# Kernel optimization log

Measured on AMD Instinct MI355X. Metric: run time of the kernel, lower is better.

## Reference

```python
import jax, jax.numpy as jnp
import numpy as np

B, S, D, H, MLP = 8, 1024, 768, 12, 3072
HD = D // H
EPS = 1e-5


def setup_inputs() -> dict:
    key = jax.random.key(0)
    ks = jax.random.split(key, 5)
    sd = lambda fan_in: 1.0 / np.sqrt(fan_in)
    return {
        "x": jax.random.normal(ks[0], (B, S, D), jnp.float32),
        "w_qkv": jax.random.normal(ks[1], (D, 3 * D), jnp.float32) * sd(D),
        "w_out": jax.random.normal(ks[2], (D, D), jnp.float32) * sd(D),
        "b_out": jnp.zeros((D,), jnp.float32),
        "w1": jax.random.normal(ks[3], (D, MLP), jnp.float32) * sd(D),
        "b1": jnp.zeros((MLP,), jnp.float32),
        "w2": jax.random.normal(ks[4], (MLP, D), jnp.float32) * sd(MLP),
        "b2": jnp.zeros((D,), jnp.float32),
    }


def _instance_norm(x):
    # torch InstanceNorm2d on a 3D [B,S,D] tensor treats it as unbatched (C,H,W):
    # normalize over (S, D) per batch element, biased var, eps=1e-5, no affine.
    mu = jnp.mean(x, axis=(1, 2), keepdims=True)
    var = jnp.mean(jnp.square(x - mu), axis=(1, 2), keepdims=True)
    return (x - mu) * jax.lax.rsqrt(var + EPS)


def reference(x, w_qkv, w_out, b_out, w1, b1, w2, b2):
    scale = HD ** -0.5
    # --- self-attention branch ---
    h = _instance_norm(x)
    qkv = (h @ w_qkv).reshape(B, S, 3, H, HD)          # (qkv, heads, head_dim) split
    qkv = qkv.transpose(2, 0, 3, 1, 4)                  # [3, B, H, S, HD]
    q, k, v = qkv[0], qkv[1], qkv[2]
    att = jax.nn.softmax(jnp.einsum('bhxd,bhyd->bhxy', q, k) * scale, axis=-1)
    o = jnp.einsum('bhxy,bhyd->bhxd', att, v)           # [B, H, S, HD]
    o = o.transpose(0, 2, 1, 3).reshape(B, S, D)        # b h l d -> b l (h d)
    x = x + (o @ w_out + b_out)
    # --- MLP branch (exact erf GELU, as nn.GELU default) ---
    h2 = _instance_norm(x)
    m = jax.nn.gelu(h2 @ w1 + b1, approximate=False) @ w2 + b2
    return x + m
```

## Files before the change

kernel.cpp:

```cpp
#include <hip/hip_runtime.h>
#include <hip/hip_bf16.h>

typedef __hip_bfloat16 bf16;
typedef __attribute__((ext_vector_type(8))) short short8;
typedef __attribute__((ext_vector_type(4))) float f32x4;

#define B_   8
#define S_   1024
#define D_   768
#define H_   12
#define HD_  64
#define MLP_ 3072
#define SD_  (S_ * D_)

#define QSCALE 0.18033688011112042f

__device__ __forceinline__ float b2f(short h) {
  union { unsigned u; float f; } w;
  w.u = ((unsigned)(unsigned short)h) << 16;
  return w.f;
}

__device__ __forceinline__ void gl2lds16(const bf16* g, bf16* l) {
  __builtin_amdgcn_global_load_lds(
      (const __attribute__((address_space(1))) unsigned*)(const void*)g,
      (__attribute__((address_space(3))) unsigned*)(void*)l, 16, 0, 0);
}

__global__ __launch_bounds__(256) void transpose_all(
    const float* __restrict__ w_qkv, const float* __restrict__ w_out,
    const float* __restrict__ w1, const float* __restrict__ w2,
    bf16* __restrict__ t_qkv, bf16* __restrict__ t_out,
    bf16* __restrict__ t1, bf16* __restrict__ t2) {
  const int t = blockIdx.x;
  const float* in; bf16* out; int R, C, idx;
  if (t < 1728)      { in = w_qkv; out = t_qkv; R = 768;  C = 2304; idx = t; }
  else if (t < 2304) { in = w_out; out = t_out; R = 768;  C = 768;  idx = t - 1728; }
  else if (t < 4608) { in = w1;    out = t1;    R = 768;  C = 3072; idx = t - 2304; }
  else               { in = w2;    out = t2;    R = 3072; C = 768;  idx = t - 4608; }
  const int nbx = C >> 5;
  const int bx = (idx % nbx) * 32, by = (idx / nbx) * 32;
  __shared__ float tt[32][33];
  const int tx = threadIdx.x & 31, ty = threadIdx.x >> 5;
#pragma unroll
  for (int rr = 0; rr < 32; rr += 8)
    tt[ty + rr][tx] = in[(long)(by + ty + rr) * C + bx + tx];
  __syncthreads();
#pragma unroll
  for (int rr = 0; rr < 32; rr += 8)
    out[(long)(bx + ty + rr) * R + by + tx] = __float2bfloat16(tt[tx][ty + rr]);
}

__global__ __launch_bounds__(256) void stats_partial(const float* __restrict__ x,
                                                     float* __restrict__ redp,
                                                     const bf16* __restrict__ wt1,
                                                     const bf16* __restrict__ wt_qkv,
                                                     float* __restrict__ cs1,
                                                     float* __restrict__ csq,
                                                     bf16* __restrict__ xb) {
  if (blockIdx.x >= 768) {
    const bf16* wsrc; float* cdst; int bi;
    if (blockIdx.x < 816) { wsrc = wt1;    cdst = cs1; bi = blockIdx.x - 768; }
    else                  { wsrc = wt_qkv; cdst = csq; bi = blockIdx.x - 816; }
    const int row = bi * 64 + (threadIdx.x >> 2);
    const int part = threadIdx.x & 3;
    const bf16* wr = wsrc + (long)row * 768 + part * 192;
    float s = 0.f;
#pragma unroll
    for (int u = 0; u < 24; ++u) {
      short8 v = *(const short8*)(wr + u * 8);
#pragma unroll
      for (int e = 0; e < 8; ++e) s += b2f(v[e]);
    }
    s += __shfl_xor(s, 1, 64);
    s += __shfl_xor(s, 2, 64);
    if (part == 0) cdst[row] = s;
    return;
  }
  const long off = (long)blockIdx.x * 8192;
  float s = 0.f, s2 = 0.f;
#pragma unroll
  for (int it = 0; it < 4; ++it) {
    const long i = off + ((long)threadIdx.x + it * 256) * 8;
    float4 v0 = *(const float4*)(x + i);
    float4 v1 = *(const float4*)(x + i + 4);
    s += v0.x + v0.y + v0.z + v0.w + v1.x + v1.y + v1.z + v1.w;
    s2 += v0.x * v0.x + v0.y * v0.y + v0.z * v0.z + v0.w * v0.w +
          v1.x * v1.x + v1.y * v1.y + v1.z * v1.z + v1.w * v1.w;
    __align__(16) bf16 tmp[8];
    tmp[0] = __float2bfloat16(v0.x); tmp[1] = __float2bfloat16(v0.y);
    tmp[2] = __float2bfloat16(v0.z); tmp[3] = __float2bfloat16(v0.w);
    tmp[4] = __float2bfloat16(v1.x); tmp[5] = __float2bfloat16(v1.y);
    tmp[6] = __float2bfloat16(v1.z); tmp[7] = __float2bfloat16(v1.w);
    *(short8*)(xb + i) = *(const short8*)tmp;
  }
#pragma unroll
  for (int o = 1; o < 64; o <<= 1) { s += __shfl_xor(s, o, 64); s2 += __shfl_xor(s2, o, 64); }
  __shared__ float sh[8];
  const int wave = threadIdx.x >> 6, lane = threadIdx.x & 63;
  if (lane == 0) { sh[wave * 2] = s; sh[wave * 2 + 1] = s2; }
  __syncthreads();
  if (threadIdx.x == 0) {
    redp[blockIdx.x * 2]     = sh[0] + sh[2] + sh[4] + sh[6];
    redp[blockIdx.x * 2 + 1] = sh[1] + sh[3] + sh[5] + sh[7];
  }
}

__global__ __launch_bounds__(512) void stats_final(const float* __restrict__ redp,
                                                   float* __restrict__ red_x,
                                                   float* __restrict__ red2) {
  const int b = threadIdx.x >> 6, lane = threadIdx.x & 63;
  const int i0 = (b * 96 + lane) * 2;
  float s  = redp[i0]     + ((lane < 32) ? redp[i0 + 128]     : 0.f);
  float s2 = redp[i0 + 1] + ((lane < 32) ? redp[i0 + 128 + 1] : 0.f);
#pragma unroll
  for (int o = 1; o < 64; o <<= 1) { s += __shfl_xor(s, o, 64); s2 += __shfl_xor(s2, o, 64); }
  if (lane == 0) { red_x[b * 2] = s; red_x[b * 2 + 1] = s2; }
  if (threadIdx.x < 16) red2[threadIdx.x] = 0.f;
}

template <int EPI, bool STATS>
__global__ __launch_bounds__(256) void gemm_k(
    const bf16* __restrict__ A, const bf16* __restrict__ Bt,
    int M, int N, int K,
    const float* __restrict__ biasf, const float* __restrict__ resf,
    const float* __restrict__ cs, const float* __restrict__ stat_in,
    float* __restrict__ outf,
    bf16* __restrict__ outb0, bf16* __restrict__ outb1, bf16* __restrict__ outb2,
    float* __restrict__ statp) {
  __shared__ __align__(16) bf16 As[128 * 64];
  __shared__ __align__(16) bf16 Bs[128 * 64];
  __shared__ float sred[8];
  const int tid = threadIdx.x;
  const int bm = blockIdx.x * 128, bn = blockIdx.y * 128;
  const int wave = tid >> 6, lane = tid & 63;
  const int quad = lane >> 4, l16 = lane & 15;
  const int wm = (wave >> 1) * 64, wn = (wave & 1) * 64;
  const int swz = l16 & 7;

  f32x4 acc[4][4];
#pragma unroll
  for (int i = 0; i < 4; ++i)
#pragma unroll
    for (int j = 0; j < 4; ++j) acc[i][j] = (f32x4){0.f, 0.f, 0.f, 0.f};

  const int srow = tid >> 3;
  const int sgc = (tid & 7) ^ (srow & 7);
  const bf16* Ab = A + (long)(bm + srow) * K + sgc * 8;
  const bf16* Bb = Bt + (long)(bn + srow) * K + sgc * 8;

  auto stage = [&](int k0) {
#pragma unroll
    for (int s = 0; s < 4; ++s)
      gl2lds16(Ab + (long)(s * 32) * K + k0, &As[0] + s * 2048 + tid * 8);
#pragma unroll
    for (int s = 0; s < 4; ++s)
      gl2lds16(Bb + (long)(s * 32) * K + k0, &Bs[0] + s * 2048 + tid * 8);
  };

  stage(0);
  const int nk = K >> 6;
  for (int kt = 0; kt < nk; ++kt) {
    __syncthreads();
    short8 a[2][4], b[2][4];
#pragma unroll
    for (int kk = 0; kk < 2; ++kk) {
      const int co = ((kk * 4 + quad) ^ swz) * 8;
#pragma unroll
      for (int i = 0; i < 4; ++i)
        a[kk][i] = *(const short8*)(&As[0] + (wm + i * 16 + l16) * 64 + co);
#pragma unroll
      for (int j = 0; j < 4; ++j)
        b[kk][j] = *(const short8*)(&Bs[0] + (wn + j * 16 + l16) * 64 + co);
    }
    __syncthreads();
    if (kt + 1 < nk) stage((kt + 1) * 64);
#pragma unroll
    for (int kk = 0; kk < 2; ++kk)
#pragma unroll
      for (int i = 0; i < 4; ++i)
#pragma unroll
        for (int j = 0; j < 4; ++j)
          acc[i][j] = __builtin_amdgcn_mfma_f32_16x16x32_bf16(a[kk][i], b[kk][j], acc[i][j], 0, 0, 0);
  }

  const int m0 = bm + wm + quad * 4;
  const int n0 = bn + wn + l16;
  const int batch = bm >> 10;
  float mu = 0.f, rs = 0.f;
  if (EPI == 0 || EPI == 2) {
    const float s1 = stat_in[batch * 2], s2v = stat_in[batch * 2 + 1];
    mu = s1 * (1.0f / SD_);
    rs = rsqrtf(s2v * (1.0f / SD_) - mu * mu + 1e-5f);
  }
  float ts = 0.f, ts2 = 0.f;
#pragma unroll
  for (int i = 0; i < 4; ++i) {
#pragma unroll
    for (int j = 0; j < 4; ++j) {
      const int n = n0 + j * 16;
#pragma unroll
      for (int r = 0; r < 4; ++r) {
        const int m = m0 + i * 16 + r;
        float v = acc[i][j][r];
        if (EPI == 0) {
          v = rs * (v - mu * cs[n]);
          const int t = n / D_;
          const int rr2 = n - t * D_;
          const int hh = rr2 >> 6, dd = rr2 & 63;
          const int bb = m >> 10, ss = m & 1023;
          const long hoff = (long)(bb * H_ + hh);
          if (t == 0)      outb0[(hoff * S_ + ss) * HD_ + dd] = __float2bfloat16(v * QSCALE);
          else if (t == 1) outb1[(hoff * S_ + ss) * HD_ + dd] = __float2bfloat16(v);
          else             outb2[(hoff * HD_ + dd) * S_ + ss] = __float2bfloat16(v);
        } else if (EPI == 1) {
          v += biasf[n] + resf[(long)m * N + n];
          outf[(long)m * N + n] = v;
          outb0[(long)m * N + n] = __float2bfloat16(v);
          if (STATS) { ts += v; ts2 += v * v; }
        } else if (EPI == 2) {
          v = rs * (v - mu * cs[n]) + biasf[n];
          float u = v * v;
          float y = v * (1.0f + 0.044715f * u) * 0.7978845608028654f;
          float z = exp2f(y * -2.885390081777927f);
          v = v * __builtin_amdgcn_rcpf(1.0f + z);
          outb0[(long)m * N + n] = __float2bfloat16(v);
        } else {
          v += biasf[n] + resf[(long)m * N + n];
          outf[(long)m * N + n] = v;
        }
      }
    }
  }
  if (STATS) {
#pragma unroll
    for (int o = 1; o < 64; o <<= 1) { ts += __shfl_xor(ts, o, 64); ts2 += __shfl_xor(ts2, o, 64); }
    if (lane == 0) { sred[wave * 2] = ts; sred[wave * 2 + 1] = ts2; }
    __syncthreads();
    if (tid == 0) {
      atomicAdd(&statp[batch * 2], sred[0] + sred[2] + sred[4] + sred[6]);
      atomicAdd(&statp[batch * 2 + 1], sred[1] + sred[3] + sred[5] + sred[7]);
    }
  }
}

__global__ __launch_bounds__(256) void attn64(const bf16* __restrict__ q,
                                              const bf16* __restrict__ k,
                                              const bf16* __restrict__ vt,
                                              bf16* __restrict__ o) {
  __shared__ __align__(16) bf16 Ks[2][64 * 64];
  __shared__ __align__(16) bf16 Vs[2][64 * 64];
  __shared__ __align__(16) bf16 Ps[4 * 16 * 64];
  const int bh = blockIdx.x, qt = blockIdx.y;
  const int tid = threadIdx.x, wave = tid >> 6, lane = tid & 63;
  const int quad = lane >> 4, l16 = lane & 15;
  const int sw = (l16 & 7) ^ ((l16 >> 3) & 1);
  const long base = (long)bh * (S_ * HD_);
  const bf16* kg = k + base;
  const bf16* vg = vt + base;

  const int srow = tid >> 3;
  const int scg = (tid & 7) ^ (srow & 7) ^ ((srow >> 3) & 1);

  short8 aq[2];
#pragma unroll
  for (int kk = 0; kk < 2; ++kk)
    aq[kk] = *(const short8*)(q + base + (long)(qt * 64 + wave * 16 + l16) * HD_ +
                              kk * 32 + quad * 8);

  gl2lds16(kg + (long)srow * HD_ + scg * 8, &Ks[0][0] + tid * 8);
  gl2lds16(kg + (long)(32 + srow) * HD_ + scg * 8, &Ks[0][0] + 2048 + tid * 8);
  gl2lds16(vg + (long)srow * S_ + scg * 8, &Vs[0][0] + tid * 8);
  gl2lds16(vg + (long)(32 + srow) * S_ + scg * 8, &Vs[0][0] + 2048 + tid * 8);

  f32x4 oacc[4];
#pragma unroll
  for (int j = 0; j < 4; ++j) oacc[j] = (f32x4){0.f, 0.f, 0.f, 0.f};
  float lp = 0.f;

  for (int c = 0; c < 16; ++c) {
    const int cur = c & 1;
    __syncthreads();

    f32x4 s[4];
#pragma unroll
    for (int i = 0; i < 4; ++i) s[i] = (f32x4){0.f, 0.f, 0.f, 0.f};
#pragma unroll
    for (int kk = 0; kk < 2; ++kk) {
#pragma unroll
      for (int i = 0; i < 4; ++i) {
        short8 ak = *(const short8*)(&Ks[cur][0] + (i * 16 + l16) * 64 +
                                     (((kk * 4 + quad) ^ sw) * 8));
        s[i] = __builtin_amdgcn_mfma_f32_16x16x32_bf16(ak, aq[kk], s[i], 0, 0, 0);
      }
    }

    if (c < 15) {
      const int nxt = cur ^ 1;
      gl2lds16(kg + (long)((c + 1) * 64 + srow) * HD_ + scg * 8, &Ks[nxt][0] + tid * 8);
      gl2lds16(kg + (long)((c + 1) * 64 + 32 + srow) * HD_ + scg * 8, &Ks[nxt][0] + 2048 + tid * 8);
      gl2lds16(vg + (long)srow * S_ + (c + 1) * 64 + scg * 8, &Vs[nxt][0] + tid * 8);
      gl2lds16(vg + (long)(32 + srow) * S_ + (c + 1) * 64 + scg * 8, &Vs[nxt][0] + 2048 + tid * 8);
    }

#pragma unroll
    for (int i = 0; i < 4; ++i) {
      __align__(8) bf16 pk[4];
#pragma unroll
      for (int r = 0; r < 4; ++r) {
        float p = exp2f(s[i][r]);
        lp += p;
        pk[r] = __float2bfloat16(p);
      }
      const int chunk = 2 * i + (quad >> 1);
      *(uint2*)(Ps + wave * 1024 + l16 * 64 + ((chunk ^ sw) * 8) + (quad & 1) * 4) =
          *(const uint2*)pk;
    }

#pragma unroll
    for (int kk = 0; kk < 2; ++kk) {
      short8 ap = *(const short8*)(Ps + wave * 1024 + l16 * 64 +
                                   (((kk * 4 + quad) ^ sw) * 8));
#pragma unroll
      for (int dj = 0; dj < 4; ++dj) {
        short8 bv = *(const short8*)(&Vs[cur][0] + (dj * 16 + l16) * 64 +
                                     (((kk * 4 + quad) ^ sw) * 8));
        oacc[dj] = __builtin_amdgcn_mfma_f32_16x16x32_bf16(ap, bv, oacc[dj], 0, 0, 0);
      }
    }
  }

  float lt = lp;
  lt += __shfl_xor(lt, 16, 64);
  lt += __shfl_xor(lt, 32, 64);

  const int b = bh / H_, hh = bh - b * H_;
#pragma unroll
  for (int r = 0; r < 4; ++r) {
    const float inv = 1.0f / __shfl(lt, quad * 4 + r, 64);
    const int sg = qt * 64 + wave * 16 + quad * 4 + r;
    const long rowoff = ((long)b * S_ + sg) * D_ + hh * HD_;
#pragma unroll
    for (int dj = 0; dj < 4; ++dj)
      o[rowoff + dj * 16 + l16] = __float2bfloat16(oacc[dj][r] * inv);
  }
}

extern "C" void kernel_launch(void* const* d_in, const int* in_sizes, int n_in,
                              void* d_out, int out_size, void* d_ws, size_t ws_size,
                              hipStream_t stream) {
  const float* x     = (const float*)d_in[0];
  const float* w_qkv = (const float*)d_in[1];
  const float* w_out = (const float*)d_in[2];
  const float* b_out = (const float*)d_in[3];
  const float* w1    = (const float*)d_in[4];
  const float* b1    = (const float*)d_in[5];
  const float* w2    = (const float*)d_in[6];
  const float* b2    = (const float*)d_in[7];
  float* out = (float*)d_out;

  bf16* wt_qkv = (bf16*)d_ws;
  bf16* wt_out = wt_qkv + 2304 * 768;
  bf16* wt1    = wt_out + 768 * 768;
  bf16* wt2    = wt1 + 3072 * 768;
  bf16* qb     = wt2 + 768 * 3072;
  bf16* kb     = qb + 6291456;
  bf16* vtb    = kb + 6291456;
  bf16* ob     = vtb + 6291456;
  float* x1f   = (float*)(ob + 6291456);
  bf16* hb     = (bf16*)(x1f + 6291456);
  float* redp  = (float*)(hb + 6291456);
  float* red_x = redp + 1536;
  float* red2  = red_x + 16;
  float* cs1   = red2 + 16;
  float* csq   = cs1 + 3072;
  bf16* gb     = qb;
  bf16* xb     = hb;
  bf16* x1b    = hb;

  transpose_all<<<6912, 256, 0, stream>>>(w_qkv, w_out, w1, w2,
                                          wt_qkv, wt_out, wt1, wt2);

  stats_partial<<<768 + 48 + 36, 256, 0, stream>>>(x, redp, wt1, wt_qkv,
                                                   cs1, csq, xb);
  stats_final<<<1, 512, 0, stream>>>(redp, red_x, red2);

  gemm_k<0, false><<<dim3(64, 18), 256, 0, stream>>>(
      xb, wt_qkv, 8192, 2304, 768, nullptr, nullptr, csq, red_x,
      nullptr, qb, kb, vtb, nullptr);
  attn64<<<dim3(B_ * H_, 16), 256, 0, stream>>>(qb, kb, vtb, ob);

  gemm_k<1, true><<<dim3(64, 6), 256, 0, stream>>>(
      ob, wt_out, 8192, 768, 768, b_out, x, nullptr, nullptr,
      x1f, x1b, nullptr, nullptr, red2);

  gemm_k<2, false><<<dim3(64, 24), 256, 0, stream>>>(
      x1b, wt1, 8192, 3072, 768, b1, nullptr, cs1, red2,
      nullptr, gb, nullptr, nullptr, nullptr);

  gemm_k<3, false><<<dim3(64, 6), 256, 0, stream>>>(
      gb, wt2, 8192, 768, 3072, b2, x1f, nullptr, nullptr,
      out, nullptr, nullptr, nullptr, nullptr);
}
```

Measured before the change: 345.8 us.

## Grow attention blocks to 128 query rows with 512 threads sharing K/V tiles

The attention kernel now runs 8 waves per block over 128 query rows instead of 4 waves over 64, so each K/V tile staged in LDS is reused by twice as many waves. That halves global K/V traffic and the number of blocks. Each thread now issues one LDS prefetch per tile instead of two. The loop is manually unrolled by two with constant double-buffer indices and running pointers to cut address arithmetic. The cost is a larger LDS footprint (the P buffer doubles) and fewer blocks (768), which may reduce latency hiding on this GPU.

```diff
diff --git a/kernel.cpp b/kernel.cpp
--- a/kernel.cpp
+++ b/kernel.cpp
@@ -244,13 +244,13 @@
   }
 }
 
-__global__ __launch_bounds__(256) void attn64(const bf16* __restrict__ q,
+__global__ __launch_bounds__(512) void attn64(const bf16* __restrict__ q,
                                               const bf16* __restrict__ k,
                                               const bf16* __restrict__ vt,
                                               bf16* __restrict__ o) {
   __shared__ __align__(16) bf16 Ks[2][64 * 64];
   __shared__ __align__(16) bf16 Vs[2][64 * 64];
-  __shared__ __align__(16) bf16 Ps[4 * 16 * 64];
+  __shared__ __align__(16) bf16 Ps[8 * 16 * 64];
   const int bh = blockIdx.x, qt = blockIdx.y;
   const int tid = threadIdx.x, wave = tid >> 6, lane = tid & 63;
   const int quad = lane >> 4, l16 = lane & 15;
@@ -265,70 +265,72 @@
   short8 aq[2];
 #pragma unroll
   for (int kk = 0; kk < 2; ++kk)
-    aq[kk] = *(const short8*)(q + base + (long)(qt * 64 + wave * 16 + l16) * HD_ +
+    aq[kk] = *(const short8*)(q + base + (long)(qt * 128 + wave * 16 + l16) * HD_ +
                               kk * 32 + quad * 8);
 
   gl2lds16(kg + (long)srow * HD_ + scg * 8, &Ks[0][0] + tid * 8);
-  gl2lds16(kg + (long)(32 + srow) * HD_ + scg * 8, &Ks[0][0] + 2048 + tid * 8);
   gl2lds16(vg + (long)srow * S_ + scg * 8, &Vs[0][0] + tid * 8);
-  gl2lds16(vg + (long)(32 + srow) * S_ + scg * 8, &Vs[0][0] + 2048 + tid * 8);
+
+  const bf16* kp = kg + (long)(64 + srow) * HD_ + scg * 8;
+  const bf16* vp = vg + (long)srow * S_ + 64 + scg * 8;
 
   f32x4 oacc[4];
 #pragma unroll
   for (int j = 0; j < 4; ++j) oacc[j] = (f32x4){0.f, 0.f, 0.f, 0.f};
   float lp = 0.f;
 
-  for (int c = 0; c < 16; ++c) {
-    const int cur = c & 1;
-    __syncthreads();
-
-    f32x4 s[4];
-#pragma unroll
-    for (int i = 0; i < 4; ++i) s[i] = (f32x4){0.f, 0.f, 0.f, 0.f};
-#pragma unroll
-    for (int kk = 0; kk < 2; ++kk) {
-#pragma unroll
-      for (int i = 0; i < 4; ++i) {
-        short8 ak = *(const short8*)(&Ks[cur][0] + (i * 16 + l16) * 64 +
-                                     (((kk * 4 + quad) ^ sw) * 8));
-        s[i] = __builtin_amdgcn_mfma_f32_16x16x32_bf16(ak, aq[kk], s[i], 0, 0, 0);
-      }
-    }
-
-    if (c < 15) {
-      const int nxt = cur ^ 1;
-      gl2lds16(kg + (long)((c + 1) * 64 + srow) * HD_ + scg * 8, &Ks[nxt][0] + tid * 8);
-      gl2lds16(kg + (long)((c + 1) * 64 + 32 + srow) * HD_ + scg * 8, &Ks[nxt][0] + 2048 + tid * 8);
-      gl2lds16(vg + (long)srow * S_ + (c + 1) * 64 + scg * 8, &Vs[nxt][0] + tid * 8);
-      gl2lds16(vg + (long)(32 + srow) * S_ + (c + 1) * 64 + scg * 8, &Vs[nxt][0] + 2048 + tid * 8);
-    }
-
-#pragma unroll
-    for (int i = 0; i < 4; ++i) {
-      __align__(8) bf16 pk[4];
-#pragma unroll
-      for (int r = 0; r < 4; ++r) {
-        float p = exp2f(s[i][r]);
-        lp += p;
-        pk[r] = __float2bfloat16(p);
-      }
-      const int chunk = 2 * i + (quad >> 1);
-      *(uint2*)(Ps + wave * 1024 + l16 * 64 + ((chunk ^ sw) * 8) + (quad & 1) * 4) =
-          *(const uint2*)pk;
-    }
-
-#pragma unroll
-    for (int kk = 0; kk < 2; ++kk) {
-      short8 ap = *(const short8*)(Ps + wave * 1024 + l16 * 64 +
-                                   (((kk * 4 + quad) ^ sw) * 8));
-#pragma unroll
-      for (int dj = 0; dj < 4; ++dj) {
-        short8 bv = *(const short8*)(&Vs[cur][0] + (dj * 16 + l16) * 64 +
-                                     (((kk * 4 + quad) ^ sw) * 8));
-        oacc[dj] = __builtin_amdgcn_mfma_f32_16x16x32_bf16(ap, bv, oacc[dj], 0, 0, 0);
-      }
-    }
-  }
+  bf16* Pw = Ps + wave * 1024 + l16 * 64;
+
+#define ATTN_STEP(CUR, DOPREF)                                                 \
+  {                                                                            \
+    __syncthreads();                                                           \
+    f32x4 s[4];                                                                \
+    _Pragma("unroll")                                                          \
+    for (int i = 0; i < 4; ++i) s[i] = (f32x4){0.f, 0.f, 0.f, 0.f};            \
+    _Pragma("unroll")                                                          \
+    for (int kk = 0; kk < 2; ++kk) {                                           \
+      _Pragma("unroll")                                                        \
+      for (int i = 0; i < 4; ++i) {                                            \
+        short8 ak = *(const short8*)(&Ks[CUR][0] + (i * 16 + l16) * 64 +       \
+                                     (((kk * 4 + quad) ^ sw) * 8));            \
+        s[i] = __builtin_amdgcn_mfma_f32_16x16x32_bf16(ak, aq[kk], s[i], 0, 0, 0); \
+      }                                                                        \
+    }                                                                          \
+    if (DOPREF) {                                                              \
+      gl2lds16(kp, &Ks[(CUR) ^ 1][0] + tid * 8);                               \
+      gl2lds16(vp, &Vs[(CUR) ^ 1][0] + tid * 8);                               \
+      kp += 64 * HD_;                                                          \
+      vp += 64;                                                                \
+    }                                                                          \
+    _Pragma("unroll")                                                          \
+    for (int i = 0; i < 4; ++i) {                                              \
+      __align__(8) bf16 pk[4];                                                 \
+      _Pragma("unroll")                                                        \
+      for (int r = 0; r < 4; ++r) {                                            \
+        float p = exp2f(s[i][r]);                                              \
+        lp += p;                                                               \
+        pk[r] = __float2bfloat16(p);                                           \
+      }                                                                        \
+      *(uint2*)(Pw + (((2 * i + (quad >> 1)) ^ sw) * 8) + (quad & 1) * 4) =    \
+          *(const uint2*)pk;                                                   \
+    }                                                                          \
+    _Pragma("unroll")                                                          \
+    for (int kk = 0; kk < 2; ++kk) {                                           \
+      short8 ap = *(const short8*)(Pw + (((kk * 4 + quad) ^ sw) * 8));         \
+      _Pragma("unroll")                                                        \
+      for (int dj = 0; dj < 4; ++dj) {                                         \
+        short8 bv = *(const short8*)(&Vs[CUR][0] + (dj * 16 + l16) * 64 +      \
+                                     (((kk * 4 + quad) ^ sw) * 8));            \
+        oacc[dj] = __builtin_amdgcn_mfma_f32_16x16x32_bf16(ap, bv, oacc[dj], 0, 0, 0); \
+      }                                                                        \
+    }                                                                          \
+  }
+
+  for (int c = 0; c < 16; c += 2) {
+    ATTN_STEP(0, true)
+    ATTN_STEP(1, (c < 14))
+  }
+#undef ATTN_STEP
 
   float lt = lp;
   lt += __shfl_xor(lt, 16, 64);
@@ -338,7 +340,7 @@
 #pragma unroll
   for (int r = 0; r < 4; ++r) {
     const float inv = 1.0f / __shfl(lt, quad * 4 + r, 64);
-    const int sg = qt * 64 + wave * 16 + quad * 4 + r;
+    const int sg = qt * 128 + wave * 16 + quad * 4 + r;
     const long rowoff = ((long)b * S_ + sg) * D_ + hh * HD_;
 #pragma unroll
     for (int dj = 0; dj < 4; ++dj)
@@ -388,7 +390,7 @@
   gemm_k<0, false><<<dim3(64, 18), 256, 0, stream>>>(
       xb, wt_qkv, 8192, 2304, 768, nullptr, nullptr, csq, red_x,
       nullptr, qb, kb, vtb, nullptr);
-  attn64<<<dim3(B_ * H_, 16), 256, 0, stream>>>(qb, kb, vtb, ob);
+  attn64<<<dim3(B_ * H_, 8), 512, 0, stream>>>(qb, kb, vtb, ob);
 
   gemm_k<1, true><<<dim3(64, 6), 256, 0, stream>>>(
       ob, wt_out, 8192, 768, 768, b_out, x, nullptr, nullptr,
```

New measurement: 333.7 us. -3.5%, faster.
